# Optimization experiments

Measured on AMD Instinct MI355X. Metric: run time of the kernel, lower is better.

## Reference

```python
import jax, jax.numpy as jnp
import numpy as np

INPUT_SIZE = 64
HIDDEN = 512
BATCH = 256
SEQ = 512

def _rnn_layer(x, W_ih, W_hh, b_ih, b_hh):
    # x: (B, T, D_in). PyTorch RNN step: h_t = tanh(x_t W_ih^T + b_ih + h_{t-1} W_hh^T + b_hh)
    B = x.shape[0]
    # precompute input projections for all timesteps: (B, T, H)
    xp = jnp.einsum('btd,hd->bth', x, W_ih) + b_ih + b_hh
    h0 = jnp.zeros((B, W_hh.shape[0]), dtype=x.dtype)

    def step(h, xp_t):
        h_new = jnp.tanh(xp_t + h @ W_hh.T)
        return h_new, h_new

    _, hs = jax.lax.scan(step, h0, jnp.swapaxes(xp, 0, 1))  # hs: (T, B, H)
    return jnp.swapaxes(hs, 0, 1)  # (B, T, H)

def setup_inputs() -> dict:
    key = jax.random.key(0)
    ks = jax.random.split(key, 11)
    s_in = 1.0 / np.sqrt(HIDDEN)
    u = lambda k, shape: jax.random.uniform(k, shape, jnp.float32, -s_in, s_in)
    return {
        'x': jax.random.normal(ks[0], (BATCH, SEQ, INPUT_SIZE), jnp.float32),
        'W_ih0': u(ks[1], (HIDDEN, INPUT_SIZE)),
        'W_hh0': u(ks[2], (HIDDEN, HIDDEN)),
        'b_ih0': u(ks[3], (HIDDEN,)),
        'b_hh0': u(ks[4], (HIDDEN,)),
        'W_ih1': u(ks[5], (HIDDEN, HIDDEN)),
        'W_hh1': u(ks[6], (HIDDEN, HIDDEN)),
        'b_ih1': u(ks[7], (HIDDEN,)),
        'b_hh1': u(ks[8], (HIDDEN,)),
        'W_fc': u(ks[9], (1, HIDDEN)),
        'b_fc': u(ks[10], (1,)),
    }

def reference(x, W_ih0, W_hh0, b_ih0, b_hh0, W_ih1, W_hh1, b_ih1, b_hh1, W_fc, b_fc):
    h1 = _rnn_layer(x, W_ih0, W_hh0, b_ih0, b_hh0)   # (B, T, H)
    h2 = _rnn_layer(h1, W_ih1, W_hh1, b_ih1, b_hh1)  # (B, T, H)
    last = h2[:, -1, :]                              # (B, H)
    return last @ W_fc.T + b_fc                      # (B, 1)
```

## Files before the change

### kernel.cpp

```cpp
#include <hip/hip_runtime.h>
#include <hip/hip_fp16.h>


typedef _Float16 h2 __attribute__((ext_vector_type(2)));
typedef _Float16 h8 __attribute__((ext_vector_type(8)));
typedef float    f4 __attribute__((ext_vector_type(4)));

#define HID   512
#define TSEQ  512
#define NB    256
#define NWAVE 8
#define NAG   32
#define NVG   14
#define NREGF (NAG + NVG)
#define NLDSF 18

#define MFMA_A(accv, av, bv) \
  asm("v_mfma_f32_16x16x32_f16 %0, %1, %2, %0" : "+v"(accv) : "v"(av), "a"(bv))
#define MFMA_V(accv, av, bv) \
  asm("v_mfma_f32_16x16x32_f16 %0, %1, %2, %0" : "+v"(accv) : "v"(av), "v"(bv))

#if __has_builtin(__builtin_amdgcn_rcpf)
#define FAST_RCP(x) __builtin_amdgcn_rcpf(x)
#else
#define FAST_RCP(x) (1.0f / (x))
#endif

static const size_t OFF_P   = 0;
static const size_t OFF_B0  = 134217728;
static const size_t OFF_B1  = OFF_B0 + 65536;
static const size_t OFF_R0  = OFF_B1 + 524288;
static const size_t OFF_L0  = OFF_R0 + 376832;
static const size_t OFF_R1  = OFF_L0 + 147456;
static const size_t OFF_L1  = OFF_R1 + 376832;
static const size_t OFF_BS0 = OFF_L1 + 147456;
static const size_t OFF_BS1 = OFF_BS0 + 2048;

__global__ void bias_kernel(const float* __restrict__ bih0, const float* __restrict__ bhh0,
                            const float* __restrict__ bih1, const float* __restrict__ bhh1,
                            float* __restrict__ bias0, float* __restrict__ bias1) {
  int i = threadIdx.x;
  bias0[i] = bih0[i] + bhh0[i];
  bias1[i] = bih1[i] + bhh1[i];
}

__global__ void cvt_half_kernel(const float* __restrict__ in, _Float16* __restrict__ outp, int n) {
  int i = blockIdx.x * 256 + threadIdx.x;
  if (i < n) outp[i] = (_Float16)in[i];
}

__global__ void pack_rec_kernel(const float* __restrict__ W, uint4* __restrict__ BregP,
                                uint4* __restrict__ BldsP) {
  int t = blockIdx.x * 256 + threadIdx.x;
  int l  = t & 63;
  int g  = (t >> 6) & 3;
  int kk = (t >> 8) & 15;
  int w  = (t >> 12) & 7;
  int n  = 64 * w + 16 * g + (l & 15);
  int k0 = 32 * kk + ((l >> 4) & 3) * 8;
  const float* src = W + (size_t)n * HID + k0;
  h8 v;
#pragma unroll
  for (int i = 0; i < 8; ++i) v[i] = (_Float16)src[i];
  uint4 u = __builtin_bit_cast(uint4, v);
  if (g < 2) {
    BregP[(w * NREGF + 2 * kk + g) * 64 + l] = u;
  } else if (g == 2) {
    if (kk < 14) BregP[(w * NREGF + NAG + kk) * 64 + l] = u;
    else         BldsP[(w * NLDSF + 16 + (kk - 14)) * 64 + l] = u;
  } else {
    BldsP[(w * NLDSF + kk) * 64 + l] = u;
  }
}

template <typename AT, int K>
__global__ __launch_bounds__(256, 2) void proj_kernel(const AT* A, const _Float16* __restrict__ Bw,
                                                      _Float16* C, const float* __restrict__ bias) {
  __shared__ _Float16 At[64][40];
  __shared__ _Float16 Bt[512][40];
  const int tid = threadIdx.x;
  const int m0 = blockIdx.x * 64;
  const int wv = tid >> 6;
  const int l = tid & 63;
  const int n0 = wv * 128;
  const int lm = l & 15;
  const int lq = l >> 4;

  f4 acc[4][8];
#pragma unroll
  for (int i = 0; i < 4; ++i)
#pragma unroll
    for (int j = 0; j < 8; ++j) acc[i][j] = (f4){0.f, 0.f, 0.f, 0.f};

  const int arow = tid >> 2;
  const int kq = (tid & 3) * 8;

  for (int k0 = 0; k0 < K; k0 += 32) {
    if (sizeof(AT) == 4) {
      const float* ap = (const float*)A + (size_t)(m0 + arow) * K + k0 + kq;
      h8 v;
#pragma unroll
      for (int i = 0; i < 8; ++i) v[i] = (_Float16)ap[i];
      *(h8*)&At[arow][kq] = v;
    } else {
      *(h8*)&At[arow][kq] = *(const h8*)((const _Float16*)A + (size_t)(m0 + arow) * K + k0 + kq);
    }
#pragma unroll
    for (int rr = 0; rr < 8; ++rr) {
      int rrow = arow + rr * 64;
      *(h8*)&Bt[rrow][kq] = *(const h8*)(Bw + (size_t)rrow * K + k0 + kq);
    }
    __syncthreads();
    h8 af[4];
#pragma unroll
    for (int mm = 0; mm < 4; ++mm) af[mm] = *(const h8*)&At[mm * 16 + lm][lq * 8];
#pragma unroll
    for (int nn = 0; nn < 8; ++nn) {
      h8 bf = *(const h8*)&Bt[n0 + nn * 16 + lm][lq * 8];
#pragma unroll
      for (int mm = 0; mm < 4; ++mm)
        acc[mm][nn] = __builtin_amdgcn_mfma_f32_16x16x32_f16(af[mm], bf, acc[mm][nn], 0, 0, 0);
    }
    __syncthreads();
  }
#pragma unroll
  for (int nn = 0; nn < 8; ++nn) {
    int col = n0 + nn * 16 + lm;
    float bv = bias[col];
#pragma unroll
    for (int mm = 0; mm < 4; ++mm) {
#pragma unroll
      for (int r = 0; r < 4; ++r) {
        int row = m0 + mm * 16 + lq * 4 + r;
        C[(size_t)row * HID + col] = (_Float16)(acc[mm][nn][r] + bv);
      }
    }
  }
}

template <bool WRITE_H, bool DO_FC>
__global__ __launch_bounds__(512, 2) void rec_kernel(
    const _Float16* __restrict__ P, _Float16* __restrict__ Pout,
    const uint4* __restrict__ BregP, const uint4* __restrict__ BldsP,
    const float* __restrict__ Wfc, const float* __restrict__ bfc, float* __restrict__ out) {
  __shared__ __align__(16) uint4 Blds[NWAVE * NLDSF * 64];
  __shared__ __align__(16) _Float16 hbuf[2][HID];
  __shared__ float red[NWAVE];
  const int tid = threadIdx.x;
  const int b = blockIdx.x;
  const int w = tid >> 6, l = tid & 63, lq = l >> 4;

  h8 breg_a[NAG];
#pragma unroll
  for (int i = 0; i < NAG; ++i)
    breg_a[i] = __builtin_bit_cast(h8, BregP[(w * NREGF + i) * 64 + l]);
  h8 breg_v[NVG];
#pragma unroll
  for (int i = 0; i < NVG; ++i)
    breg_v[i] = __builtin_bit_cast(h8, BregP[(w * NREGF + NAG + i) * 64 + l]);
#pragma unroll
  for (int j = 0; j < NLDSF; ++j)
    Blds[(w * NLDSF + j) * 64 + l] = BldsP[(w * NLDSF + j) * 64 + l];

  ((unsigned short*)hbuf[0])[tid] = 0;
  __syncthreads();

  const _Float16* prow = P + (size_t)b * TSEQ * HID;
  unsigned short xp_cur = *(const unsigned short*)(prow + tid);
  float lv = 0.f;

#pragma unroll 1
  for (int t = 0; t < TSEQ; ++t) {
    int tn = (t + 1 < TSEQ) ? t + 1 : t;
    unsigned short xp_next = *(const unsigned short*)(prow + (size_t)tn * HID + tid);
    const _Float16* hb = hbuf[t & 1];

    f4 acc[4];
#pragma unroll
    for (int g = 0; g < 4; ++g) acc[g] = (f4){0.f, 0.f, 0.f, 0.f};

#pragma unroll
    for (int kk = 0; kk < 16; ++kk) {
      h8 a = *(const h8*)(hb + kk * 32 + lq * 8);
      MFMA_A(acc[0], a, breg_a[2 * kk]);
      MFMA_A(acc[1], a, breg_a[2 * kk + 1]);
      if (kk < 14) {
        MFMA_V(acc[2], a, breg_v[kk]);
      } else {
        h8 bf = __builtin_bit_cast(h8, Blds[(w * NLDSF + 16 + (kk - 14)) * 64 + l]);
        MFMA_V(acc[2], a, bf);
      }
      {
        h8 bf = __builtin_bit_cast(h8, Blds[(w * NLDSF + kk) * 64 + l]);
        MFMA_V(acc[3], a, bf);
      }
    }

    float hr = (lq == 0) ? acc[0][0]
             : (lq == 1) ? acc[1][0]
             : (lq == 2) ? acc[2][0]
                         : acc[3][0];

    float sum = hr + (float)__builtin_bit_cast(_Float16, xp_cur);
    float ev = __expf(2.0f * sum);
    float v = 1.0f - 2.0f * FAST_RCP(ev + 1.0f);
    lv = v;
    _Float16 hw = (_Float16)v;
    *(_Float16*)(&hbuf[(t + 1) & 1][tid]) = hw;
    if (WRITE_H)
      *(Pout + (size_t)b * TSEQ * HID + (size_t)t * HID + tid) = hw;
    __syncthreads();
    xp_cur = xp_next;
  }

  if (DO_FC) {
    float fc = lv * Wfc[tid];
#pragma unroll
    for (int off = 32; off; off >>= 1) fc += __shfl_down(fc, off, 64);
    if (l == 0) red[w] = fc;
    __syncthreads();
    if (tid == 0) {
      float s = bfc[0];
#pragma unroll
      for (int i = 0; i < NWAVE; ++i) s += red[i];
      out[b] = s;
    }
  }
}

extern "C" void kernel_launch(void* const* d_in, const int* in_sizes, int n_in,
                              void* d_out, int out_size, void* d_ws, size_t ws_size,
                              hipStream_t stream) {
  const float* x    = (const float*)d_in[0];
  const float* Wih0 = (const float*)d_in[1];
  const float* Whh0 = (const float*)d_in[2];
  const float* bih0 = (const float*)d_in[3];
  const float* bhh0 = (const float*)d_in[4];
  const float* Wih1 = (const float*)d_in[5];
  const float* Whh1 = (const float*)d_in[6];
  const float* bih1 = (const float*)d_in[7];
  const float* bhh1 = (const float*)d_in[8];
  const float* Wfc  = (const float*)d_in[9];
  const float* bfc  = (const float*)d_in[10];
  float* out = (float*)d_out;
  char* ws = (char*)d_ws;

  _Float16* P  = (_Float16*)(ws + OFF_P);
  _Float16* B0 = (_Float16*)(ws + OFF_B0);
  _Float16* B1 = (_Float16*)(ws + OFF_B1);
  uint4* R0 = (uint4*)(ws + OFF_R0);
  uint4* L0 = (uint4*)(ws + OFF_L0);
  uint4* R1 = (uint4*)(ws + OFF_R1);
  uint4* L1 = (uint4*)(ws + OFF_L1);
  float* bias0 = (float*)(ws + OFF_BS0);
  float* bias1 = (float*)(ws + OFF_BS1);

  bias_kernel<<<1, 512, 0, stream>>>(bih0, bhh0, bih1, bhh1, bias0, bias1);
  cvt_half_kernel<<<128, 256, 0, stream>>>(Wih0, B0, 512 * 64);
  cvt_half_kernel<<<1024, 256, 0, stream>>>(Wih1, B1, 512 * 512);
  pack_rec_kernel<<<128, 256, 0, stream>>>(Whh0, R0, L0);
  pack_rec_kernel<<<128, 256, 0, stream>>>(Whh1, R1, L1);

  proj_kernel<float, 64><<<2048, 256, 0, stream>>>(x, B0, P, bias0);
  rec_kernel<true, false><<<NB, 512, 0, stream>>>(P, P, R0, L0, nullptr, nullptr, nullptr);
  proj_kernel<_Float16, 512><<<2048, 256, 0, stream>>>(P, B1, P, bias1);
  rec_kernel<false, true><<<NB, 512, 0, stream>>>(P, nullptr, R1, L1, Wfc, bfc, out);
}
```

Baseline: 1.493 ms.

## Use four waves per recurrent block, each computing 128 hidden columns

The recurrent kernel now runs 256 threads (4 waves) per batch row instead of 512. Each wave computes 128 output columns with 8 MFMA accumulators, and each thread finishes two hidden units per step. The weight packing is redistributed so more of W_hh stays in registers (64 AGPR plus 40 VGPR fragments) and less in LDS. The aim is to cut per-step barrier cost across fewer waves and reduce LDS weight traffic. The cost is a longer serial MFMA chain per wave, which adds latency to each timestep, and high register pressure at occupancy 1.

```diff
diff --git a/kernel.cpp b/kernel.cpp
--- a/kernel.cpp
+++ b/kernel.cpp
@@ -2,18 +2,17 @@
 #include <hip/hip_fp16.h>
 
 
-typedef _Float16 h2 __attribute__((ext_vector_type(2)));
 typedef _Float16 h8 __attribute__((ext_vector_type(8)));
 typedef float    f4 __attribute__((ext_vector_type(4)));
 
 #define HID   512
 #define TSEQ  512
 #define NB    256
-#define NWAVE 8
-#define NAG   32
-#define NVG   14
-#define NREGF (NAG + NVG)
-#define NLDSF 18
+#define NW    4
+#define NAGF  64
+#define NVGF  40
+#define NREGF (NAGF + NVGF)
+#define NLDSF 24
 
 #define MFMA_A(accv, av, bv) \
   asm("v_mfma_f32_16x16x32_f16 %0, %1, %2, %0" : "+v"(accv) : "v"(av), "a"(bv))
@@ -30,10 +29,10 @@
 static const size_t OFF_B0  = 134217728;
 static const size_t OFF_B1  = OFF_B0 + 65536;
 static const size_t OFF_R0  = OFF_B1 + 524288;
-static const size_t OFF_L0  = OFF_R0 + 376832;
-static const size_t OFF_R1  = OFF_L0 + 147456;
-static const size_t OFF_L1  = OFF_R1 + 376832;
-static const size_t OFF_BS0 = OFF_L1 + 147456;
+static const size_t OFF_L0  = OFF_R0 + 425984;
+static const size_t OFF_R1  = OFF_L0 + 98304;
+static const size_t OFF_L1  = OFF_R1 + 425984;
+static const size_t OFF_BS0 = OFF_L1 + 98304;
 static const size_t OFF_BS1 = OFF_BS0 + 2048;
 
 __global__ void bias_kernel(const float* __restrict__ bih0, const float* __restrict__ bhh0,
@@ -53,23 +52,27 @@
                                 uint4* __restrict__ BldsP) {
   int t = blockIdx.x * 256 + threadIdx.x;
   int l  = t & 63;
-  int g  = (t >> 6) & 3;
-  int kk = (t >> 8) & 15;
-  int w  = (t >> 12) & 7;
-  int n  = 64 * w + 16 * g + (l & 15);
+  int g  = (t >> 6) & 7;
+  int kk = (t >> 9) & 15;
+  int w  = (t >> 13) & 3;
+  int n  = 128 * w + 16 * g + (l & 15);
   int k0 = 32 * kk + ((l >> 4) & 3) * 8;
   const float* src = W + (size_t)n * HID + k0;
   h8 v;
 #pragma unroll
   for (int i = 0; i < 8; ++i) v[i] = (_Float16)src[i];
   uint4 u = __builtin_bit_cast(uint4, v);
-  if (g < 2) {
-    BregP[(w * NREGF + 2 * kk + g) * 64 + l] = u;
-  } else if (g == 2) {
-    if (kk < 14) BregP[(w * NREGF + NAG + kk) * 64 + l] = u;
-    else         BldsP[(w * NLDSF + 16 + (kk - 14)) * 64 + l] = u;
+  if (g < 4) {
+    BregP[(w * NREGF + 4 * kk + g) * 64 + l] = u;
+  } else if (g == 4) {
+    BregP[(w * NREGF + NAGF + kk) * 64 + l] = u;
+  } else if (g == 5) {
+    BregP[(w * NREGF + NAGF + 16 + kk) * 64 + l] = u;
+  } else if (g == 6) {
+    if (kk < 8) BregP[(w * NREGF + NAGF + 32 + kk) * 64 + l] = u;
+    else        BldsP[(w * NLDSF + (kk - 8)) * 64 + l] = u;
   } else {
-    BldsP[(w * NLDSF + kk) * 64 + l] = u;
+    BldsP[(w * NLDSF + 8 + kk) * 64 + l] = u;
   }
 }
 
@@ -139,82 +142,103 @@
 }
 
 template <bool WRITE_H, bool DO_FC>
-__global__ __launch_bounds__(512, 2) void rec_kernel(
+__global__ __launch_bounds__(256, 1) void rec_kernel(
     const _Float16* __restrict__ P, _Float16* __restrict__ Pout,
     const uint4* __restrict__ BregP, const uint4* __restrict__ BldsP,
     const float* __restrict__ Wfc, const float* __restrict__ bfc, float* __restrict__ out) {
-  __shared__ __align__(16) uint4 Blds[NWAVE * NLDSF * 64];
+  __shared__ __align__(16) uint4 Blds[NW * NLDSF * 64];
   __shared__ __align__(16) _Float16 hbuf[2][HID];
-  __shared__ float red[NWAVE];
+  __shared__ float red[NW];
   const int tid = threadIdx.x;
   const int b = blockIdx.x;
-  const int w = tid >> 6, l = tid & 63, lq = l >> 4;
-
-  h8 breg_a[NAG];
-#pragma unroll
-  for (int i = 0; i < NAG; ++i)
+  const int w = tid >> 6, l = tid & 63, lq = l >> 4, lm = l & 15;
+
+  h8 breg_a[NAGF];
+#pragma unroll
+  for (int i = 0; i < NAGF; ++i)
     breg_a[i] = __builtin_bit_cast(h8, BregP[(w * NREGF + i) * 64 + l]);
-  h8 breg_v[NVG];
-#pragma unroll
-  for (int i = 0; i < NVG; ++i)
-    breg_v[i] = __builtin_bit_cast(h8, BregP[(w * NREGF + NAG + i) * 64 + l]);
+  h8 breg_v[NVGF];
+#pragma unroll
+  for (int i = 0; i < NVGF; ++i)
+    breg_v[i] = __builtin_bit_cast(h8, BregP[(w * NREGF + NAGF + i) * 64 + l]);
 #pragma unroll
   for (int j = 0; j < NLDSF; ++j)
     Blds[(w * NLDSF + j) * 64 + l] = BldsP[(w * NLDSF + j) * 64 + l];
 
-  ((unsigned short*)hbuf[0])[tid] = 0;
+  ((unsigned int*)hbuf)[tid] = 0;
   __syncthreads();
 
+  const int col1 = 128 * w + 16 * lq + lm;
+  const int col2 = col1 + 64;
+
   const _Float16* prow = P + (size_t)b * TSEQ * HID;
-  unsigned short xp_cur = *(const unsigned short*)(prow + tid);
-  float lv = 0.f;
+  unsigned short xp1c = *(const unsigned short*)(prow + col1);
+  unsigned short xp2c = *(const unsigned short*)(prow + col2);
+  float lv1 = 0.f, lv2 = 0.f;
 
 #pragma unroll 1
   for (int t = 0; t < TSEQ; ++t) {
     int tn = (t + 1 < TSEQ) ? t + 1 : t;
-    unsigned short xp_next = *(const unsigned short*)(prow + (size_t)tn * HID + tid);
+    unsigned short xp1n = *(const unsigned short*)(prow + (size_t)tn * HID + col1);
+    unsigned short xp2n = *(const unsigned short*)(prow + (size_t)tn * HID + col2);
     const _Float16* hb = hbuf[t & 1];
 
-    f4 acc[4];
-#pragma unroll
-    for (int g = 0; g < 4; ++g) acc[g] = (f4){0.f, 0.f, 0.f, 0.f};
+    f4 acc[8];
+#pragma unroll
+    for (int g = 0; g < 8; ++g) acc[g] = (f4){0.f, 0.f, 0.f, 0.f};
 
 #pragma unroll
     for (int kk = 0; kk < 16; ++kk) {
       h8 a = *(const h8*)(hb + kk * 32 + lq * 8);
-      MFMA_A(acc[0], a, breg_a[2 * kk]);
-      MFMA_A(acc[1], a, breg_a[2 * kk + 1]);
-      if (kk < 14) {
-        MFMA_V(acc[2], a, breg_v[kk]);
+      MFMA_A(acc[0], a, breg_a[4 * kk + 0]);
+      MFMA_A(acc[1], a, breg_a[4 * kk + 1]);
+      MFMA_A(acc[2], a, breg_a[4 * kk + 2]);
+      MFMA_A(acc[3], a, breg_a[4 * kk + 3]);
+      MFMA_V(acc[4], a, breg_v[kk]);
+      MFMA_V(acc[5], a, breg_v[16 + kk]);
+      if (kk < 8) {
+        MFMA_V(acc[6], a, breg_v[32 + kk]);
       } else {
-        h8 bf = __builtin_bit_cast(h8, Blds[(w * NLDSF + 16 + (kk - 14)) * 64 + l]);
-        MFMA_V(acc[2], a, bf);
+        h8 bf = __builtin_bit_cast(h8, Blds[(w * NLDSF + (kk - 8)) * 64 + l]);
+        MFMA_V(acc[6], a, bf);
       }
       {
-        h8 bf = __builtin_bit_cast(h8, Blds[(w * NLDSF + kk) * 64 + l]);
-        MFMA_V(acc[3], a, bf);
+        h8 bf = __builtin_bit_cast(h8, Blds[(w * NLDSF + 8 + kk) * 64 + l]);
+        MFMA_V(acc[7], a, bf);
       }
     }
 
-    float hr = (lq == 0) ? acc[0][0]
-             : (lq == 1) ? acc[1][0]
-             : (lq == 2) ? acc[2][0]
-                         : acc[3][0];
-
-    float sum = hr + (float)__builtin_bit_cast(_Float16, xp_cur);
-    float ev = __expf(2.0f * sum);
-    float v = 1.0f - 2.0f * FAST_RCP(ev + 1.0f);
-    lv = v;
-    _Float16 hw = (_Float16)v;
-    *(_Float16*)(&hbuf[(t + 1) & 1][tid]) = hw;
-    if (WRITE_H)
-      *(Pout + (size_t)b * TSEQ * HID + (size_t)t * HID + tid) = hw;
-    __syncthreads();
-    xp_cur = xp_next;
+    float hr1 = (lq == 0) ? acc[0][0]
+              : (lq == 1) ? acc[1][0]
+              : (lq == 2) ? acc[2][0]
+                          : acc[3][0];
+    float hr2 = (lq == 0) ? acc[4][0]
+              : (lq == 1) ? acc[5][0]
+              : (lq == 2) ? acc[6][0]
+                          : acc[7][0];
+
+    float s1 = hr1 + (float)__builtin_bit_cast(_Float16, xp1c);
+    float s2 = hr2 + (float)__builtin_bit_cast(_Float16, xp2c);
+    float e1 = __expf(2.0f * s1);
+    float e2 = __expf(2.0f * s2);
+    float v1 = 1.0f - 2.0f * FAST_RCP(e1 + 1.0f);
+    float v2 = 1.0f - 2.0f * FAST_RCP(e2 + 1.0f);
+    lv1 = v1; lv2 = v2;
+    _Float16 hw1 = (_Float16)v1, hw2 = (_Float16)v2;
+    _Float16* hn = hbuf[(t + 1) & 1];
+    hn[col1] = hw1;
+    hn[col2] = hw2;
+    if (WRITE_H) {
+      _Float16* po = Pout + (size_t)b * TSEQ * HID + (size_t)t * HID;
+      po[col1] = hw1;
+      po[col2] = hw2;
+    }
+    __syncthreads();
+    xp1c = xp1n; xp2c = xp2n;
   }
 
   if (DO_FC) {
-    float fc = lv * Wfc[tid];
+    float fc = lv1 * Wfc[col1] + lv2 * Wfc[col2];
 #pragma unroll
     for (int off = 32; off; off >>= 1) fc += __shfl_down(fc, off, 64);
     if (l == 0) red[w] = fc;
@@ -222,7 +246,7 @@
     if (tid == 0) {
       float s = bfc[0];
 #pragma unroll
-      for (int i = 0; i < NWAVE; ++i) s += red[i];
+      for (int i = 0; i < NW; ++i) s += red[i];
       out[b] = s;
     }
   }
@@ -262,7 +286,7 @@
   pack_rec_kernel<<<128, 256, 0, stream>>>(Whh1, R1, L1);
 
   proj_kernel<float, 64><<<2048, 256, 0, stream>>>(x, B0, P, bias0);
-  rec_kernel<true, false><<<NB, 512, 0, stream>>>(P, P, R0, L0, nullptr, nullptr, nullptr);
+  rec_kernel<true, false><<<NB, 256, 0, stream>>>(P, P, R0, L0, nullptr, nullptr, nullptr);
   proj_kernel<_Float16, 512><<<2048, 256, 0, stream>>>(P, B1, P, bias1);
-  rec_kernel<false, true><<<NB, 512, 0, stream>>>(P, nullptr, R1, L1, Wfc, bfc, out);
-}
+  rec_kernel<false, true><<<NB, 256, 0, stream>>>(P, nullptr, R1, L1, Wfc, bfc, out);
+}
```

New measurement: 1.659 ms. +11.1%, slower.
